# Performance work log

Hardware: AMD Instinct MI355X
Metric: run time of the kernel (lower is better)

## Reference

```python
import jax, jax.numpy as jnp
import numpy as np

B, H, NI, NT, D = 512, 1, 36, 50, 1024
NEG = -1e9
EPS = 1e-8

def setup_inputs() -> dict:
    key = jax.random.key(0)
    ks = jax.random.split(key, 12)
    s = 1.0 / np.sqrt(D)
    return {
        "imgE": jax.random.normal(ks[0], (B, H, NI, D), jnp.float32),
        "txtE": jax.random.normal(ks[1], (B, H, NT, D), jnp.float32),
        "x_mask": jax.random.randint(ks[2], (B, H, 1, NI), 0, 2).astype(bool),
        "y_mask": jax.random.randint(ks[3], (B, H, 1, NT), 0, 2).astype(bool),
        "W_img": jax.random.uniform(ks[4], (D, D), jnp.float32, -s, s),
        "b_img": jax.random.uniform(ks[5], (D,), jnp.float32, -s, s),
        "W_txt": jax.random.uniform(ks[6], (D, D), jnp.float32, -s, s),
        "b_txt": jax.random.uniform(ks[7], (D,), jnp.float32, -s, s),
        "W_img1": jax.random.uniform(ks[8], (D, D), jnp.float32, -s, s),
        "b_img1": jax.random.uniform(ks[9], (D,), jnp.float32, -s, s),
        "W_txt1": jax.random.uniform(ks[10], (D, D), jnp.float32, -s, s),
        "b_txt1": jax.random.uniform(ks[11], (D,), jnp.float32, -s, s),
    }

def reference(imgE, txtE, x_mask, y_mask,
              W_img, b_img, W_txt, b_txt, W_img1, b_img1, W_txt1, b_txt1):
    # projections
    x = jnp.einsum('bhnd,de->bhne', imgE, W_img) + b_img   # [B,H,NI,D]
    y = jnp.einsum('bhmd,de->bhme', txtE, W_txt) + b_txt   # [B,H,NT,D]
    # cosine-normalized attention scores [B,H,NI,NT]
    att = jnp.einsum('bhnd,bhmd->bhnm', x, y)
    wx = jnp.linalg.norm(x, axis=-1)[..., :, None]          # [B,H,NI,1]
    wy = jnp.linalg.norm(y, axis=-1)[..., None, :]          # [B,H,1,NT]
    att = att / jnp.maximum(wx * wy, EPS)
    # img <- txt direction
    att1 = jax.nn.softmax(jnp.where(y_mask, NEG, att), axis=-1)
    att_x = jnp.einsum('bhnm,bhmd->bhnd', att1, txtE)
    gate_x = jax.nn.sigmoid(att_x * imgE)
    fuse_x = jnp.einsum('bhnd,de->bhne', gate_x * att_x, W_img1) + b_img1
    img_out = fuse_x + imgE
    # txt <- img direction
    att2 = jax.nn.softmax(jnp.where(x_mask, NEG, jnp.swapaxes(att, 2, 3)), axis=-1)
    att_y = jnp.einsum('bhmn,bhnd->bhmd', att2, imgE)
    gate_y = jax.nn.sigmoid(att_y * txtE)
    fuse_y = jnp.einsum('bhmd,de->bhme', gate_y * att_y, W_txt1) + b_txt1
    txt_out = fuse_y + txtE
    return (img_out, txt_out)
```

## Files before the change

kernel.cpp:

```cpp
#include <hip/hip_runtime.h>

typedef unsigned short u16;
typedef unsigned int u32;
typedef __attribute__((ext_vector_type(8))) short sv8;
typedef __attribute__((ext_vector_type(4))) float fv4;

__device__ __forceinline__ u16 f2b(float f) {
  u32 u = __builtin_bit_cast(u32, f);
  u32 r = (u + 0x7fffu + ((u >> 16) & 1u)) >> 16;
  return (u16)r;
}
__device__ __forceinline__ float b2f(u16 h) {
  return __builtin_bit_cast(float, ((u32)h) << 16);
}
__device__ __forceinline__ void gld16(const void* g, void* l) {
  __builtin_amdgcn_global_load_lds(
      (const __attribute__((address_space(1))) u32*)g,
      (__attribute__((address_space(3))) u32*)l, 16, 0, 0);
}

__global__ __launch_bounds__(256) void cast_k(const float4* __restrict__ in,
                                              u16* __restrict__ out, int n4) {
  int i = blockIdx.x * 256 + threadIdx.x;
  const int stride = gridDim.x * 256;
  for (; i < n4; i += stride) {
    float4 v = in[i];
    u32 p0 = (u32)f2b(v.x) | ((u32)f2b(v.y) << 16);
    u32 p1 = (u32)f2b(v.z) | ((u32)f2b(v.w) << 16);
    uint2 o; o.x = p0; o.y = p1;
    ((uint2*)out)[i] = o;
  }
}

__global__ __launch_bounds__(256) void wtrans_k(const float* __restrict__ W0,
                                                const float* __restrict__ W1,
                                                const float* __restrict__ W2,
                                                const float* __restrict__ W3,
                                                u16* __restrict__ out) {
  const int z = blockIdx.z;
  const float* W = (z == 0) ? W0 : (z == 1) ? W1 : (z == 2) ? W2 : W3;
  u16* o = out + (size_t)z * 1048576;
  __shared__ float t[32][33];
  const int tid = threadIdx.x;
  const int r = tid >> 5, cc = tid & 31;
  const int d0 = blockIdx.x * 32, e0 = blockIdx.y * 32;
#pragma unroll
  for (int i = 0; i < 4; ++i)
    t[r + i * 8][cc] = W[(size_t)(d0 + r + i * 8) * 1024 + e0 + cc];
  __syncthreads();
#pragma unroll
  for (int i = 0; i < 4; ++i) {
    int row = r + i * 8;
    o[(size_t)(e0 + row) * 1024 + d0 + cc] = f2b(t[cc][row]);
  }
}

template <int MODE>
__global__ __launch_bounds__(256, 2) void gemm2_k(
    const u16* __restrict__ Aimg, const u16* __restrict__ Atxt,
    const u16* __restrict__ Wimg, const u16* __restrict__ Wtxt,
    const float* __restrict__ bii, const float* __restrict__ btt,
    const float* __restrict__ rii, const float* __restrict__ rtt,
    u16* __restrict__ obi, u16* __restrict__ obt,
    float* __restrict__ ofi, float* __restrict__ oft) {
  __shared__ __attribute__((aligned(16))) char smem[65536];
  const int tid = threadIdx.x;
  const int lane = tid & 63;
  const int w = tid >> 6;
  const int l15 = lane & 15, l4 = lane >> 4;
  const int lin = blockIdx.y * 8 + blockIdx.x;
  const int xcd = lin & 7, slot = lin >> 3;
  const int bcol0 = (slot & 7) * 128;
  const int prow = xcd + ((slot >> 3) << 3);

  const char* Ab; const char* Bb; const float* bias; const float* resid;
  u16* ob; float* of; int brow0;
  if (prow < 144) {
    brow0 = prow * 128;
    Ab = (const char*)Aimg + (size_t)brow0 * 2048;
    Bb = (const char*)Wimg + (size_t)bcol0 * 2048;
    bias = bii; resid = rii; ob = obi; of = ofi;
  } else {
    brow0 = (prow - 144) * 128;
    Ab = (const char*)Atxt + (size_t)brow0 * 2048;
    Bb = (const char*)Wtxt + (size_t)bcol0 * 2048;
    bias = btt; resid = rtt; ob = obt; of = oft;
  }
  const int wr = (w >> 1) * 64;
  const int wc = (w & 1) * 64;
  fv4 acc[4][4] = {};

  const int srow = tid >> 3;
  const int schunk = tid & 7;

  auto STAGE = [&](int bb, int k0) {
#pragma unroll
    for (int i = 0; i < 4; ++i) {
      int row = i * 32 + srow;
      int g = schunk ^ (row & 7);
      gld16(Ab + (size_t)row * 2048 + k0 * 2 + g * 16,
            smem + bb * 32768 + i * 4096 + tid * 16);
    }
#pragma unroll
    for (int i = 0; i < 4; ++i) {
      int row = i * 32 + srow;
      int g = schunk ^ (row & 7);
      gld16(Bb + (size_t)row * 2048 + k0 * 2 + g * 16,
            smem + bb * 32768 + 16384 + i * 4096 + tid * 16);
    }
  };

  STAGE(0, 0);
  int cur = 0;
  for (int t = 0; t < 16; ++t) {
    if (t < 15) {
      STAGE(cur ^ 1, (t + 1) * 64);
      asm volatile("s_waitcnt vmcnt(8)" ::: "memory");
    } else {
      asm volatile("s_waitcnt vmcnt(0)" ::: "memory");
    }
    __builtin_amdgcn_s_barrier();
    __builtin_amdgcn_sched_barrier(0);
    const char* Al = smem + cur * 32768;
    const char* Bl = Al + 16384;
#pragma unroll
    for (int ks = 0; ks < 2; ++ks) {
      sv8 af[4], bf[4];
#pragma unroll
      for (int m = 0; m < 4; ++m) {
        int row = wr + m * 16 + l15;
        int c = (ks * 4 + l4) ^ (row & 7);
        af[m] = *(const sv8*)(Al + row * 128 + c * 16);
      }
#pragma unroll
      for (int n = 0; n < 4; ++n) {
        int row = wc + n * 16 + l15;
        int c = (ks * 4 + l4) ^ (row & 7);
        bf[n] = *(const sv8*)(Bl + row * 128 + c * 16);
      }
#pragma unroll
      for (int m = 0; m < 4; ++m)
#pragma unroll
        for (int n = 0; n < 4; ++n)
          acc[m][n] = __builtin_amdgcn_mfma_f32_16x16x32_bf16(af[m], bf[n], acc[m][n], 0, 0, 0);
    }
    __builtin_amdgcn_sched_barrier(0);
    __builtin_amdgcn_s_barrier();
    cur ^= 1;
  }

#pragma unroll
  for (int n = 0; n < 4; ++n) {
    const int col = bcol0 + wc + n * 16 + l15;
    const float bv = bias[col];
#pragma unroll
    for (int m = 0; m < 4; ++m) {
      fv4 v = acc[m][n];
#pragma unroll
      for (int j = 0; j < 4; ++j) {
        const int row = brow0 + wr + m * 16 + l4 * 4 + j;
        const size_t idx = (size_t)row * 1024 + col;
        float r = v[j] + bv;
        if (MODE == 0) ob[idx] = f2b(r);
        else           of[idx] = r + resid[idx];
      }
    }
  }
}

__global__ __launch_bounds__(512) void score_k(const u16* __restrict__ Xb,
                                               const u16* __restrict__ Yb,
                                               const void* __restrict__ xmask,
                                               const void* __restrict__ ymask,
                                               float* __restrict__ P1g,
                                               float* __restrict__ P2g) {
  __shared__ float attL[48 * 65];
  __shared__ float wxL[88];
  __shared__ unsigned char msk[88];
  const int b = blockIdx.x;
  const int tid = threadIdx.x;
  const int w = tid >> 6, lane = tid & 63;
  const int l15 = lane & 15, l4 = lane >> 4;

  u32 det = 0;
  {
    const u32* mm = (const u32*)xmask;
#pragma unroll
    for (int i = 0; i < 16; ++i) det |= mm[i * 4];
    det |= mm[1] | mm[2] | mm[3];
  }
  const bool m_i32 = (det <= 1u);
  if (tid < 36)
    msk[tid] = (unsigned char)(m_i32 ? (((const int*)xmask)[b * 36 + tid] != 0)
                                     : (((const unsigned char*)xmask)[b * 36 + tid] != 0));
  if (tid >= 64 && tid < 114) {
    int m = tid - 64;
    msk[36 + m] = (unsigned char)(m_i32 ? (((const int*)ymask)[b * 50 + m] != 0)
                                        : (((const unsigned char*)ymask)[b * 50 + m] != 0));
  }

  const u16* Xr = Xb + (size_t)b * 36864;
  const u16* Yr = Yb + (size_t)b * 51200;

  if (w < 4) {
#pragma unroll
    for (int sweep = 0; sweep < 3; ++sweep) {
      int r = sweep * 32 + (tid >> 3);
      int j = tid & 7;
      if (r < 86) {
        const u32* p = (const u32*)((r < 36) ? (Xr + r * 1024)
                                             : (Yr + (size_t)(r - 36) * 1024)) + j * 64;
        float s = 0.f;
#pragma unroll
        for (int i = 0; i < 16; ++i) {
          uint4 q = ((const uint4*)p)[i];
          u32 qq[4] = {q.x, q.y, q.z, q.w};
#pragma unroll
          for (int k2 = 0; k2 < 4; ++k2) {
            float lo = __builtin_bit_cast(float, qq[k2] << 16);
            float hi = __builtin_bit_cast(float, qq[k2] & 0xffff0000u);
            s = fmaf(lo, lo, fmaf(hi, hi, s));
          }
        }
        s += __shfl_xor(s, 1); s += __shfl_xor(s, 2); s += __shfl_xor(s, 4);
        if (j == 0) wxL[r] = sqrtf(s);
      }
    }
  } else {
    const int tn = w - 4;
    fv4 ac0 = {}, ac1 = {}, ac2 = {};
    const u16* Yp = Yr + (size_t)(tn * 16 + l15) * 1024 + l4 * 8;
    const u16* Xp = Xr + (size_t)l15 * 1024 + l4 * 8;
#pragma unroll 2
    for (int ks = 0; ks < 32; ++ks) {
      sv8 bf = *(const sv8*)(Yp + ks * 32);
      sv8 a0 = *(const sv8*)(Xp + ks * 32);
      sv8 a1 = *(const sv8*)(Xp + 16 * 1024 + ks * 32);
      sv8 a2 = *(const sv8*)(Xp + 32 * 1024 + ks * 32);
      ac0 = __builtin_amdgcn_mfma_f32_16x16x32_bf16(a0, bf, ac0, 0, 0, 0);
      ac1 = __builtin_amdgcn_mfma_f32_16x16x32_bf16(a1, bf, ac1, 0, 0, 0);
      ac2 = __builtin_amdgcn_mfma_f32_16x16x32_bf16(a2, bf, ac2, 0, 0, 0);
    }
    const int col = tn * 16 + l15;
#pragma unroll
    for (int j = 0; j < 4; ++j) {
      attL[(l4 * 4 + j) * 65 + col] = ac0[j];
      attL[(16 + l4 * 4 + j) * 65 + col] = ac1[j];
      attL[(32 + l4 * 4 + j) * 65 + col] = ac2[j];
    }
  }
  __syncthreads();

#pragma unroll
  for (int sweep = 0; sweep < 2; ++sweep) {
    int R = sweep * 64 + (tid >> 3);
    int j = tid & 7;
    if (R < 36) {
      float wxn = wxL[R];
      float sv[7];
#pragma unroll
      for (int i = 0; i < 7; ++i) {
        int m = j + i * 8;
        if (m < 50) {
          float den = fmaxf(wxn * wxL[36 + m], 1e-8f);
          float v = attL[R * 65 + m] / den;
          sv[i] = msk[36 + m] ? -1e9f : v;
        } else sv[i] = -3.4e38f;
      }
      float mx = sv[0];
#pragma unroll
      for (int i = 1; i < 7; ++i) mx = fmaxf(mx, sv[i]);
      mx = fmaxf(mx, __shfl_xor(mx, 1));
      mx = fmaxf(mx, __shfl_xor(mx, 2));
      mx = fmaxf(mx, __shfl_xor(mx, 4));
      float e[7], sum = 0.f;
#pragma unroll
      for (int i = 0; i < 7; ++i) {
        e[i] = (j + i * 8 < 50) ? __expf(sv[i] - mx) : 0.f;
        sum += e[i];
      }
      sum += __shfl_xor(sum, 1); sum += __shfl_xor(sum, 2); sum += __shfl_xor(sum, 4);
      float rs = 1.f / sum;
      float* dst = P1g + ((size_t)b * 36 + R) * 64;
#pragma unroll
      for (int i = 0; i < 7; ++i) {
        int m = j + i * 8;
        if (m < 50) dst[m] = e[i] * rs;
      }
    } else if (R < 86) {
      int m = R - 36;
      float wym = wxL[R];
      float sv[5];
#pragma unroll
      for (int i = 0; i < 5; ++i) {
        int n = j + i * 8;
        if (n < 36) {
          float den = fmaxf(wxL[n] * wym, 1e-8f);
          float v = attL[n * 65 + m] / den;
          sv[i] = msk[n] ? -1e9f : v;
        } else sv[i] = -3.4e38f;
      }
      float mx = sv[0];
#pragma unroll
      for (int i = 1; i < 5; ++i) mx = fmaxf(mx, sv[i]);
      mx = fmaxf(mx, __shfl_xor(mx, 1));
      mx = fmaxf(mx, __shfl_xor(mx, 2));
      mx = fmaxf(mx, __shfl_xor(mx, 4));
      float e[5], sum = 0.f;
#pragma unroll
      for (int i = 0; i < 5; ++i) {
        e[i] = (j + i * 8 < 36) ? __expf(sv[i] - mx) : 0.f;
        sum += e[i];
      }
      sum += __shfl_xor(sum, 1); sum += __shfl_xor(sum, 2); sum += __shfl_xor(sum, 4);
      float rs = 1.f / sum;
      float* dst = P2g + ((size_t)b * 50 + m) * 64;
#pragma unroll
      for (int i = 0; i < 5; ++i) {
        int n = j + i * 8;
        if (n < 36) dst[n] = e[i] * rs;
      }
    }
  }
}

__global__ __launch_bounds__(256) void pv_k(const float* __restrict__ P1g,
                                            const float* __restrict__ P2g,
                                            const u16* __restrict__ imgA,
                                            const u16* __restrict__ txtA,
                                            u16* __restrict__ gxw,
                                            u16* __restrict__ gyw) {
  __shared__ float ldsP1[36 * 64];
  __shared__ float ldsP2[50 * 64];
  const int b = blockIdx.x & 511;
  const int d = ((blockIdx.x >> 9) << 8) + threadIdx.x;
  const int tid = threadIdx.x;

  {
    const float4* s1 = (const float4*)(P1g + (size_t)b * 2304);
    float4* l1 = (float4*)ldsP1;
    for (int i = tid; i < 576; i += 256) l1[i] = s1[i];
    const float4* s2 = (const float4*)(P2g + (size_t)b * 3200);
    float4* l2 = (float4*)ldsP2;
    for (int i = tid; i < 800; i += 256) l2[i] = s2[i];
  }

  const u16* tp = txtA + (size_t)b * 51200 + d;
  const u16* ip = imgA + (size_t)b * 36864 + d;
  float tv[50], iv[36];
#pragma unroll
  for (int m = 0; m < 50; ++m) tv[m] = b2f(tp[(size_t)m * 1024]);
#pragma unroll
  for (int n = 0; n < 36; ++n) iv[n] = b2f(ip[(size_t)n * 1024]);
  __syncthreads();

  u16* gx = gxw + (size_t)b * 36864 + d;
#pragma unroll
  for (int n = 0; n < 36; ++n) {
    const float4* pr4 = (const float4*)(ldsP1 + n * 64);
    float4 a4 = {0.f, 0.f, 0.f, 0.f};
#pragma unroll
    for (int i = 0; i < 12; ++i) {
      float4 p = pr4[i];
      a4.x = fmaf(p.x, tv[4 * i + 0], a4.x);
      a4.y = fmaf(p.y, tv[4 * i + 1], a4.y);
      a4.z = fmaf(p.z, tv[4 * i + 2], a4.z);
      a4.w = fmaf(p.w, tv[4 * i + 3], a4.w);
    }
    float acc = (a4.x + a4.y) + (a4.z + a4.w);
    acc = fmaf(ldsP1[n * 64 + 48], tv[48], acc);
    acc = fmaf(ldsP1[n * 64 + 49], tv[49], acc);
    float t = acc * iv[n];
    float g = acc / (1.f + __expf(-t));
    gx[(size_t)n * 1024] = f2b(g);
  }
  u16* gy = gyw + (size_t)b * 51200 + d;
#pragma unroll
  for (int m = 0; m < 50; ++m) {
    const float4* pr4 = (const float4*)(ldsP2 + m * 64);
    float4 a4 = {0.f, 0.f, 0.f, 0.f};
#pragma unroll
    for (int i = 0; i < 9; ++i) {
      float4 p = pr4[i];
      a4.x = fmaf(p.x, iv[4 * i + 0], a4.x);
      a4.y = fmaf(p.y, iv[4 * i + 1], a4.y);
      a4.z = fmaf(p.z, iv[4 * i + 2], a4.z);
      a4.w = fmaf(p.w, iv[4 * i + 3], a4.w);
    }
    float acc = (a4.x + a4.y) + (a4.z + a4.w);
    float t = acc * tv[m];
    float g = acc / (1.f + __expf(-t));
    gy[(size_t)m * 1024] = f2b(g);
  }
}

extern "C" void kernel_launch(void* const* d_in, const int* in_sizes, int n_in,
                              void* d_out, int out_size, void* d_ws, size_t ws_size,
                              hipStream_t stream) {
  (void)in_sizes; (void)n_in; (void)out_size; (void)ws_size;
  const float* imgE = (const float*)d_in[0];
  const float* txtE = (const float*)d_in[1];
  const void* xmask = d_in[2];
  const void* ymask = d_in[3];
  const float* W_img  = (const float*)d_in[4];
  const float* b_img  = (const float*)d_in[5];
  const float* W_txt  = (const float*)d_in[6];
  const float* b_txt  = (const float*)d_in[7];
  const float* W_img1 = (const float*)d_in[8];
  const float* b_img1 = (const float*)d_in[9];
  const float* W_txt1 = (const float*)d_in[10];
  const float* b_txt1 = (const float*)d_in[11];
  float* out_img = (float*)d_out;
  float* out_txt = out_img + (size_t)18874368;

  char* ws = (char*)d_ws;
  u16* Wt   = (u16*)(ws);
  u16* imgA = (u16*)(ws + 8388608);
  u16* txtA = (u16*)(ws + 46137344);
  u16* Xb   = (u16*)(ws + 98566144);
  u16* Yb   = (u16*)(ws + 136314880);
  float* P1g = (float*)(ws + 188743680);
  float* P2g = (float*)(ws + 193462272);
  u16* gxw  = (u16*)(ws + 98566144);
  u16* gyw  = (u16*)(ws + 136314880);

  cast_k<<<2048, 256, 0, stream>>>((const float4*)imgE, imgA, 4718592);
  cast_k<<<2048, 256, 0, stream>>>((const float4*)txtE, txtA, 6553600);
  wtrans_k<<<dim3(32, 32, 4), 256, 0, stream>>>(W_img, W_txt, W_img1, W_txt1, Wt);
  gemm2_k<0><<<dim3(8, 344), 256, 0, stream>>>(
      imgA, txtA, Wt, Wt + 1048576, b_img, b_txt, nullptr, nullptr,
      Xb, Yb, nullptr, nullptr);
  score_k<<<512, 512, 0, stream>>>(Xb, Yb, xmask, ymask, P1g, P2g);
  pv_k<<<2048, 256, 0, stream>>>(P1g, P2g, imgA, txtA, gxw, gyw);
  gemm2_k<1><<<dim3(8, 344), 256, 0, stream>>>(
      gxw, gyw, Wt + 2097152, Wt + 3145728, b_img1, b_txt1, imgE, txtE,
      nullptr, nullptr, out_img, out_txt);
}
```

Before: 425.9 us.

## Enlarge GEMM tiles to 256x256 with 8 waves and prefetch two stages ahead

Replaces the 128x128, 4-wave GEMM with a 256x256 tile computed by 512 threads, where each wave produces a 128x64 output. It uses 128 KB of LDS double buffering, issues two stages up front and reloads the next-but-one stage after the compute barrier. The block-to-XCD mapping is remapped so each XCD takes a contiguous range of tiles. The larger tile cuts global and L2 traffic per FLOP, but it doubles accumulator registers and LDS use, which lowers occupancy and leaves fewer blocks (688) to balance across CUs.

```diff
diff --git a/kernel.cpp b/kernel.cpp
--- a/kernel.cpp
+++ b/kernel.cpp
@@ -56,113 +56,108 @@
 }
 
 template <int MODE>
-__global__ __launch_bounds__(256, 2) void gemm2_k(
+__global__ __launch_bounds__(512, 2) void gemm3_k(
     const u16* __restrict__ Aimg, const u16* __restrict__ Atxt,
     const u16* __restrict__ Wimg, const u16* __restrict__ Wtxt,
     const float* __restrict__ bii, const float* __restrict__ btt,
     const float* __restrict__ rii, const float* __restrict__ rtt,
     u16* __restrict__ obi, u16* __restrict__ obt,
     float* __restrict__ ofi, float* __restrict__ oft) {
-  __shared__ __attribute__((aligned(16))) char smem[65536];
+  __shared__ __attribute__((aligned(16))) char smem[131072];
   const int tid = threadIdx.x;
   const int lane = tid & 63;
   const int w = tid >> 6;
+  const int wm = w >> 2, wn = w & 3;
   const int l15 = lane & 15, l4 = lane >> 4;
-  const int lin = blockIdx.y * 8 + blockIdx.x;
-  const int xcd = lin & 7, slot = lin >> 3;
-  const int bcol0 = (slot & 7) * 128;
-  const int prow = xcd + ((slot >> 3) << 3);
+  const int lin = blockIdx.y * 4 + blockIdx.x;
+  const int xcd = lin & 7, idx = lin >> 3;
+  const int s = xcd * 86 + idx;
+  const int bcol0 = (s & 3) * 256;
+  const int prow = s >> 2;
 
   const char* Ab; const char* Bb; const float* bias; const float* resid;
   u16* ob; float* of; int brow0;
-  if (prow < 144) {
-    brow0 = prow * 128;
+  if (prow < 72) {
+    brow0 = prow * 256;
     Ab = (const char*)Aimg + (size_t)brow0 * 2048;
     Bb = (const char*)Wimg + (size_t)bcol0 * 2048;
     bias = bii; resid = rii; ob = obi; of = ofi;
   } else {
-    brow0 = (prow - 144) * 128;
+    brow0 = (prow - 72) * 256;
     Ab = (const char*)Atxt + (size_t)brow0 * 2048;
     Bb = (const char*)Wtxt + (size_t)bcol0 * 2048;
     bias = btt; resid = rtt; ob = obt; of = oft;
   }
-  const int wr = (w >> 1) * 64;
-  const int wc = (w & 1) * 64;
-  fv4 acc[4][4] = {};
-
+
+  fv4 acc[8][4] = {};
   const int srow = tid >> 3;
   const int schunk = tid & 7;
 
   auto STAGE = [&](int bb, int k0) {
+    char* base = smem + bb * 65536;
 #pragma unroll
     for (int i = 0; i < 4; ++i) {
-      int row = i * 32 + srow;
+      int row = i * 64 + srow;
       int g = schunk ^ (row & 7);
-      gld16(Ab + (size_t)row * 2048 + k0 * 2 + g * 16,
-            smem + bb * 32768 + i * 4096 + tid * 16);
+      gld16(Ab + (size_t)row * 2048 + k0 * 2 + g * 16, base + i * 8192 + tid * 16);
     }
 #pragma unroll
     for (int i = 0; i < 4; ++i) {
-      int row = i * 32 + srow;
+      int row = i * 64 + srow;
       int g = schunk ^ (row & 7);
       gld16(Bb + (size_t)row * 2048 + k0 * 2 + g * 16,
-            smem + bb * 32768 + 16384 + i * 4096 + tid * 16);
+            base + 32768 + i * 8192 + tid * 16);
     }
   };
 
   STAGE(0, 0);
-  int cur = 0;
+  STAGE(1, 64);
   for (int t = 0; t < 16; ++t) {
-    if (t < 15) {
-      STAGE(cur ^ 1, (t + 1) * 64);
-      asm volatile("s_waitcnt vmcnt(8)" ::: "memory");
-    } else {
-      asm volatile("s_waitcnt vmcnt(0)" ::: "memory");
-    }
+    const int cur = t & 1;
+    if (t < 15) asm volatile("s_waitcnt vmcnt(8)" ::: "memory");
+    else        asm volatile("s_waitcnt vmcnt(0)" ::: "memory");
     __builtin_amdgcn_s_barrier();
     __builtin_amdgcn_sched_barrier(0);
-    const char* Al = smem + cur * 32768;
-    const char* Bl = Al + 16384;
+    const char* Tl = smem + cur * 65536;
 #pragma unroll
     for (int ks = 0; ks < 2; ++ks) {
-      sv8 af[4], bf[4];
-#pragma unroll
-      for (int m = 0; m < 4; ++m) {
-        int row = wr + m * 16 + l15;
+      sv8 bf[4];
+#pragma unroll
+      for (int n = 0; n < 4; ++n) {
+        int row = wn * 64 + n * 16 + l15;
         int c = (ks * 4 + l4) ^ (row & 7);
-        af[m] = *(const sv8*)(Al + row * 128 + c * 16);
-      }
-#pragma unroll
-      for (int n = 0; n < 4; ++n) {
-        int row = wc + n * 16 + l15;
+        bf[n] = *(const sv8*)(Tl + 32768 + row * 128 + c * 16);
+      }
+#pragma unroll
+      for (int m = 0; m < 8; ++m) {
+        int row = wm * 128 + m * 16 + l15;
         int c = (ks * 4 + l4) ^ (row & 7);
-        bf[n] = *(const sv8*)(Bl + row * 128 + c * 16);
-      }
-#pragma unroll
-      for (int m = 0; m < 4; ++m)
+        sv8 af = *(const sv8*)(Tl + row * 128 + c * 16);
 #pragma unroll
         for (int n = 0; n < 4; ++n)
-          acc[m][n] = __builtin_amdgcn_mfma_f32_16x16x32_bf16(af[m], bf[n], acc[m][n], 0, 0, 0);
+          acc[m][n] = __builtin_amdgcn_mfma_f32_16x16x32_bf16(af, bf[n], acc[m][n], 0, 0, 0);
+      }
     }
     __builtin_amdgcn_sched_barrier(0);
     __builtin_amdgcn_s_barrier();
-    cur ^= 1;
+    __builtin_amdgcn_sched_barrier(0);
+    if (t < 14) STAGE(cur, (t + 2) * 64);
   }
 
 #pragma unroll
   for (int n = 0; n < 4; ++n) {
-    const int col = bcol0 + wc + n * 16 + l15;
+    const int col = bcol0 + wn * 64 + n * 16 + l15;
     const float bv = bias[col];
 #pragma unroll
-    for (int m = 0; m < 4; ++m) {
+    for (int m = 0; m < 8; ++m) {
       fv4 v = acc[m][n];
 #pragma unroll
       for (int j = 0; j < 4; ++j) {
-        const int row = brow0 + wr + m * 16 + l4 * 4 + j;
-        const size_t idx = (size_t)row * 1024 + col;
+        const int row = brow0 + wm * 128 + m * 16 + l4 * 4 + j;
+        const size_t idx2 = (size_t)row * 1024 + col;
         float r = v[j] + bv;
-        if (MODE == 0) ob[idx] = f2b(r);
-        else           of[idx] = r + resid[idx];
+        if (MODE == 0) ob[idx2] = f2b(r);
+        else           of[idx2] = r + resid[idx2];
       }
     }
   }
@@ -427,12 +422,12 @@
   cast_k<<<2048, 256, 0, stream>>>((const float4*)imgE, imgA, 4718592);
   cast_k<<<2048, 256, 0, stream>>>((const float4*)txtE, txtA, 6553600);
   wtrans_k<<<dim3(32, 32, 4), 256, 0, stream>>>(W_img, W_txt, W_img1, W_txt1, Wt);
-  gemm2_k<0><<<dim3(8, 344), 256, 0, stream>>>(
+  gemm3_k<0><<<dim3(4, 172), 512, 0, stream>>>(
       imgA, txtA, Wt, Wt + 1048576, b_img, b_txt, nullptr, nullptr,
       Xb, Yb, nullptr, nullptr);
   score_k<<<512, 512, 0, stream>>>(Xb, Yb, xmask, ymask, P1g, P2g);
   pv_k<<<2048, 256, 0, stream>>>(P1g, P2g, imgA, txtA, gxw, gyw);
-  gemm2_k<1><<<dim3(8, 344), 256, 0, stream>>>(
+  gemm3_k<1><<<dim3(4, 172), 512, 0, stream>>>(
       gxw, gyw, Wt + 2097152, Wt + 3145728, b_img1, b_txt1, imgE, txtE,
       nullptr, nullptr, out_img, out_txt);
 }
```

After: 478.6 us. 1.12x slower.

## Halve GEMM K-tile to 32 and raise occupancy to four blocks per CU

Applied to the files above, without the earlier changes.

The projection/fusion GEMM now stages K-slices of 32 instead of 64, halving LDS use to 32KB with a matching 4-chunk XOR swizzle and 32 pipeline iterations, and raises launch bounds to 4 blocks per CU. The aim is more resident waves to hide global-load latency. The cost is twice as many barriers per tile and more register pressure under the tighter bound, which could cause spills. The epilogue loops are reordered and the residual read and output write in MODE 1 use nontemporal loads and stores.

```diff
diff --git a/kernel.cpp b/kernel.cpp
--- a/kernel.cpp
+++ b/kernel.cpp
@@ -56,14 +56,14 @@
 }
 
 template <int MODE>
-__global__ __launch_bounds__(256, 2) void gemm2_k(
+__global__ __launch_bounds__(256, 4) void gemm2_k(
     const u16* __restrict__ Aimg, const u16* __restrict__ Atxt,
     const u16* __restrict__ Wimg, const u16* __restrict__ Wtxt,
     const float* __restrict__ bii, const float* __restrict__ btt,
     const float* __restrict__ rii, const float* __restrict__ rtt,
     u16* __restrict__ obi, u16* __restrict__ obt,
     float* __restrict__ ofi, float* __restrict__ oft) {
-  __shared__ __attribute__((aligned(16))) char smem[65536];
+  __shared__ __attribute__((aligned(16))) char smem[32768];
   const int tid = threadIdx.x;
   const int lane = tid & 63;
   const int w = tid >> 6;
@@ -90,79 +90,77 @@
   const int wc = (w & 1) * 64;
   fv4 acc[4][4] = {};
 
-  const int srow = tid >> 3;
-  const int schunk = tid & 7;
-
   auto STAGE = [&](int bb, int k0) {
-#pragma unroll
-    for (int i = 0; i < 4; ++i) {
-      int row = i * 32 + srow;
-      int g = schunk ^ (row & 7);
+    char* base = smem + bb * 16384;
+#pragma unroll
+    for (int j = 0; j < 2; ++j) {
+      int row = (w * 2 + j) * 16 + (lane >> 2);
+      int g = (lane & 3) ^ ((row >> 1) & 3);
       gld16(Ab + (size_t)row * 2048 + k0 * 2 + g * 16,
-            smem + bb * 32768 + i * 4096 + tid * 16);
-    }
-#pragma unroll
-    for (int i = 0; i < 4; ++i) {
-      int row = i * 32 + srow;
-      int g = schunk ^ (row & 7);
+            base + (w * 2 + j) * 1024 + lane * 16);
+    }
+#pragma unroll
+    for (int j = 0; j < 2; ++j) {
+      int row = (w * 2 + j) * 16 + (lane >> 2);
+      int g = (lane & 3) ^ ((row >> 1) & 3);
       gld16(Bb + (size_t)row * 2048 + k0 * 2 + g * 16,
-            smem + bb * 32768 + 16384 + i * 4096 + tid * 16);
+            base + 8192 + (w * 2 + j) * 1024 + lane * 16);
     }
   };
 
   STAGE(0, 0);
-  int cur = 0;
-  for (int t = 0; t < 16; ++t) {
-    if (t < 15) {
-      STAGE(cur ^ 1, (t + 1) * 64);
-      asm volatile("s_waitcnt vmcnt(8)" ::: "memory");
+  for (int t = 0; t < 32; ++t) {
+    const int cur = t & 1;
+    if (t < 31) {
+      STAGE(cur ^ 1, (t + 1) * 32);
+      asm volatile("s_waitcnt vmcnt(4)" ::: "memory");
     } else {
       asm volatile("s_waitcnt vmcnt(0)" ::: "memory");
     }
     __builtin_amdgcn_s_barrier();
     __builtin_amdgcn_sched_barrier(0);
-    const char* Al = smem + cur * 32768;
-    const char* Bl = Al + 16384;
-#pragma unroll
-    for (int ks = 0; ks < 2; ++ks) {
-      sv8 af[4], bf[4];
-#pragma unroll
-      for (int m = 0; m < 4; ++m) {
-        int row = wr + m * 16 + l15;
-        int c = (ks * 4 + l4) ^ (row & 7);
-        af[m] = *(const sv8*)(Al + row * 128 + c * 16);
-      }
-#pragma unroll
-      for (int n = 0; n < 4; ++n) {
-        int row = wc + n * 16 + l15;
-        int c = (ks * 4 + l4) ^ (row & 7);
-        bf[n] = *(const sv8*)(Bl + row * 128 + c * 16);
-      }
-#pragma unroll
-      for (int m = 0; m < 4; ++m)
-#pragma unroll
-        for (int n = 0; n < 4; ++n)
-          acc[m][n] = __builtin_amdgcn_mfma_f32_16x16x32_bf16(af[m], bf[n], acc[m][n], 0, 0, 0);
-    }
+    const char* Tl = smem + cur * 16384;
+    sv8 af[4], bf[4];
+#pragma unroll
+    for (int m = 0; m < 4; ++m) {
+      int row = wr + m * 16 + l15;
+      int c = l4 ^ ((row >> 1) & 3);
+      af[m] = *(const sv8*)(Tl + row * 64 + c * 16);
+    }
+#pragma unroll
+    for (int n = 0; n < 4; ++n) {
+      int row = wc + n * 16 + l15;
+      int c = l4 ^ ((row >> 1) & 3);
+      bf[n] = *(const sv8*)(Tl + 8192 + row * 64 + c * 16);
+    }
+#pragma unroll
+    for (int m = 0; m < 4; ++m)
+#pragma unroll
+      for (int n = 0; n < 4; ++n)
+        acc[m][n] = __builtin_amdgcn_mfma_f32_16x16x32_bf16(af[m], bf[n], acc[m][n], 0, 0, 0);
     __builtin_amdgcn_sched_barrier(0);
     __builtin_amdgcn_s_barrier();
-    cur ^= 1;
-  }
-
-#pragma unroll
-  for (int n = 0; n < 4; ++n) {
-    const int col = bcol0 + wc + n * 16 + l15;
-    const float bv = bias[col];
-#pragma unroll
-    for (int m = 0; m < 4; ++m) {
-      fv4 v = acc[m][n];
-#pragma unroll
-      for (int j = 0; j < 4; ++j) {
-        const int row = brow0 + wr + m * 16 + l4 * 4 + j;
+  }
+
+  float bv[4];
+#pragma unroll
+  for (int n = 0; n < 4; ++n) bv[n] = bias[bcol0 + wc + n * 16 + l15];
+#pragma unroll
+  for (int m = 0; m < 4; ++m) {
+#pragma unroll
+    for (int j = 0; j < 4; ++j) {
+      const int row = brow0 + wr + m * 16 + l4 * 4 + j;
+#pragma unroll
+      for (int n = 0; n < 4; ++n) {
+        const int col = bcol0 + wc + n * 16 + l15;
         const size_t idx = (size_t)row * 1024 + col;
-        float r = v[j] + bv;
-        if (MODE == 0) ob[idx] = f2b(r);
-        else           of[idx] = r + resid[idx];
+        float r = acc[m][n][j] + bv[n];
+        if (MODE == 0) {
+          ob[idx] = f2b(r);
+        } else {
+          float rv = __builtin_nontemporal_load(&resid[idx]);
+          __builtin_nontemporal_store(r + rv, &of[idx]);
+        }
       }
     }
   }
```

Result: slower. 446.3 us (+4.8%).
